# Performance work log

Hardware: AMD Instinct MI355X
Metric: run time of the kernel (lower is better)

## Reference

```python
import jax, jax.numpy as jnp
import numpy as np

NP, NV, S, E = 1500000, 1200000, 50000, 1600000
M, D, C = 32, 64, 20
BN_EPS = 1e-4


def _bn(x, g, be):
    # eval-mode BatchNorm1d with running_mean=0, running_var=1, eps=1e-4
    return x * (g / np.float32(np.sqrt(1.0 + BN_EPS))) + be


def _head(x, W1, b1, g, be, W2, b2):
    # Linear -> BN -> ReLU -> Linear (torch Linear: y = x @ W.T + b)
    h = jax.nn.relu(_bn(x @ W1.T + b1, g, be))
    return h @ W2.T + b2


def setup_inputs() -> dict:
    keys = iter(jax.random.split(jax.random.key(0), 96))
    def nk():
        return next(keys)
    def w(out_d, in_d):
        return (jax.random.normal(nk(), (out_d, in_d), jnp.float32) / np.float32(np.sqrt(in_d)))
    def vec(n, s=0.02):
        return jax.random.normal(nk(), (n,), jnp.float32) * s
    inp = {}
    inp['output_feats'] = jax.random.normal(nk(), (NV, M), jnp.float32)
    inp['input_map'] = jax.random.randint(nk(), (NP,), 0, NV, jnp.int32)
    inp['superpoint'] = jax.random.randint(nk(), (NP,), 0, S, jnp.int32)
    inp['superpoint_center_xyz'] = jax.random.normal(nk(), (S, 3), jnp.float32)
    inp['edge_u'] = jax.random.randint(nk(), (E,), 0, S, jnp.int32)
    inp['edge_v'] = jax.random.randint(nk(), (E,), 0, S, jnp.int32)
    inp['W_ecc'] = w(D, M)
    for pref, din, dout in [('lin', M, C), ('ssem', D, C), ('soff', D, 3), ('socc', D, 1), ('ssize', D, 1), ('feat', D, 7)]:
        inp[pref + '_W1'] = w(din, din)
        inp[pref + '_b1'] = vec(din)
        inp[pref + '_g'] = 1.0 + vec(din, 0.1)
        inp[pref + '_be'] = vec(din, 0.1)
        inp[pref + '_W2'] = w(dout, din)
        inp[pref + '_b2'] = vec(dout)
    inp['pos_W1'] = w(16, 3)
    inp['pos_b1'] = vec(16)
    inp['pos_W2'] = w(1, 16)
    inp['pos_b2'] = vec(1)
    inp['Wq'] = w(D, D)
    inp['Wk'] = w(D, D)
    inp['Wv'] = w(D, D)
    return inp


def reference(output_feats, input_map, superpoint, superpoint_center_xyz, edge_u, edge_v, W_ecc,
              lin_W1, lin_b1, lin_g, lin_be, lin_W2, lin_b2,
              ssem_W1, ssem_b1, ssem_g, ssem_be, ssem_W2, ssem_b2,
              soff_W1, soff_b1, soff_g, soff_be, soff_W2, soff_b2,
              socc_W1, socc_b1, socc_g, socc_be, socc_W2, socc_b2,
              ssize_W1, ssize_b1, ssize_g, ssize_be, ssize_W2, ssize_b2,
              feat_W1, feat_b1, feat_g, feat_be, feat_W2, feat_b2,
              pos_W1, pos_b1, pos_W2, pos_b2, Wq, Wk, Wv):
    nseg = superpoint_center_xyz.shape[0]
    # voxel -> point gather
    pts = output_feats[input_map]                                   # [Np, M]
    semantic_scores = _head(pts, lin_W1, lin_b1, lin_g, lin_be, lin_W2, lin_b2)  # [Np, C]
    # scatter-mean point features into superpoint embeddings
    cnt = jax.ops.segment_sum(jnp.ones((pts.shape[0],), pts.dtype), superpoint, num_segments=nseg)
    emb = jax.ops.segment_sum(pts, superpoint, num_segments=nseg) / jnp.maximum(cnt, 1.0)[:, None]  # [S, M]
    # ECC graph network stand-in: linear projection media -> 64
    ecc = emb @ W_ecc.T                                             # [S, D]
    sp_sem = _head(ecc, ssem_W1, ssem_b1, ssem_g, ssem_be, ssem_W2, ssem_b2)      # [S, C]
    sp_off = _head(ecc, soff_W1, soff_b1, soff_g, soff_be, soff_W2, soff_b2)      # [S, 3]
    sp_occ = _head(ecc, socc_W1, socc_b1, socc_g, socc_be, socc_W2, socc_b2)[:, 0]  # [S]
    sp_size = _head(ecc, ssize_W1, ssize_b1, ssize_g, ssize_be, ssize_W2, ssize_b2)[:, 0]  # [S]
    # edge attention with segment-wise softmax over destination edge_u
    q = ecc @ Wq.T
    k = ecc @ Wk.T
    v = ecc @ Wv.T
    d = superpoint_center_xyz[edge_u] - superpoint_center_xyz[edge_v]             # [E, 3]
    pos = (jax.nn.relu(d @ pos_W1.T + pos_b1) @ pos_W2.T + pos_b2)[:, 0]          # [E]
    aff = (q[edge_u] * k[edge_v]).sum(-1) / np.float32(np.sqrt(D)) * pos          # [E]
    mx = jax.ops.segment_max(aff, edge_u, num_segments=nseg)
    ex = jnp.exp(aff - mx[edge_u])
    tot = jax.ops.segment_sum(ex, edge_u, num_segments=nseg)
    soft = ex / tot[edge_u]                                                       # [E]
    res = jax.ops.segment_sum(soft[:, None] * v[edge_v], edge_u, num_segments=nseg)  # [S, D]
    sp_feat = ecc + res
    sp_disc = _head(sp_feat, feat_W1, feat_b1, feat_g, feat_be, feat_W2, feat_b2)  # [S, 7]
    return (semantic_scores, sp_sem, sp_off, sp_occ, sp_size, soft, sp_disc)
```

## Files before the change

kernel.cpp:

```cpp
#include <hip/hip_runtime.h>
#include <hip/hip_bf16.h>

#define NP_ 1500000
#define NV_ 1200000
#define S_  50000
#define E_  1600000


__global__ void k_zero(int* a, int* b, int* c, int* d, int n) {
    int i = blockIdx.x * blockDim.x + threadIdx.x;
    if (i < n) { a[i] = 0; b[i] = 0; c[i] = 0; d[i] = 0; }
}

__global__ void k_hist2(const int* __restrict__ sp, int* __restrict__ pcnt,
                        const int* __restrict__ eu, int* __restrict__ ecnt) {
    int i = blockIdx.x * blockDim.x + threadIdx.x;
    if (i < NP_) {
        atomicAdd(&pcnt[sp[i]], 1);
    } else {
        int j = i - NP_;
        if (j < E_) atomicAdd(&ecnt[eu[j]], 1);
    }
}

__global__ void k_scan2(const int* __restrict__ pcnt, int* __restrict__ pstart,
                        const int* __restrict__ ecnt, int* __restrict__ estart) {
    __shared__ int sums[1024];
    const int* cnt = (blockIdx.x == 0) ? pcnt : ecnt;
    int* start = (blockIdx.x == 0) ? pstart : estart;
    const int n = S_;
    int t = threadIdx.x;
    int chunk = (n + 1023) / 1024;
    int lo = t * chunk;
    int hi = lo + chunk; if (hi > n) hi = n;
    int s = 0;
    for (int i = lo; i < hi; i++) s += cnt[i];
    sums[t] = s;
    __syncthreads();
    for (int off = 1; off < 1024; off <<= 1) {
        int v = (t >= off) ? sums[t - off] : 0;
        __syncthreads();
        sums[t] += v;
        __syncthreads();
    }
    int run = sums[t] - s;
    for (int i = lo; i < hi; i++) { start[i] = run; run += cnt[i]; }
    if (t == 1023) start[n] = run;
}

__global__ void k_fill2(const int* __restrict__ sp, const int* __restrict__ imap,
                        const int* __restrict__ pstart, int* __restrict__ pcur,
                        int* __restrict__ vidx,
                        const int* __restrict__ eu, const int* __restrict__ ev,
                        const int* __restrict__ estart, int* __restrict__ ecur,
                        int* __restrict__ elist, int* __restrict__ evsarr,
                        const float* __restrict__ ctr,
                        const float* __restrict__ pw1, const float* __restrict__ pb1,
                        const float* __restrict__ pw2, const float* __restrict__ pb2,
                        float* __restrict__ posv) {
    int i = blockIdx.x * blockDim.x + threadIdx.x;
    if (i < NP_) {
        int s = sp[i];
        int off = atomicAdd(&pcur[s], 1);
        vidx[pstart[s] + off] = imap[i];
    } else {
        int e = i - NP_;
        if (e < E_) {
            int u = eu[e], w = ev[e];
            int off = atomicAdd(&ecur[u], 1);
            int r = estart[u] + off;
            elist[r] = e;
            evsarr[r] = w;
            float dx = ctr[u * 3]     - ctr[w * 3];
            float dy = ctr[u * 3 + 1] - ctr[w * 3 + 1];
            float dz = ctr[u * 3 + 2] - ctr[w * 3 + 2];
            float pos = pb2[0];
            #pragma unroll
            for (int hh = 0; hh < 16; hh++) {
                float aa = pb1[hh] + dx * pw1[hh * 3] + dy * pw1[hh * 3 + 1] + dz * pw1[hh * 3 + 2];
                pos += fmaxf(aa, 0.0f) * pw2[hh];
            }
            posv[r] = pos;
        }
    }
}


__global__ __launch_bounds__(256, 4) void k_point_head(
    const float* __restrict__ feats, const int* __restrict__ imap,
    const float* __restrict__ W1, const float* __restrict__ b1,
    const float* __restrict__ g, const float* __restrict__ be,
    const float* __restrict__ W2, const float* __restrict__ b2,
    float* __restrict__ out, int n)
{
    int p = blockIdx.x * 256 + threadIdx.x;
    if (p >= n) return;
    const float4* src = (const float4*)(feats + (size_t)imap[p] * 32);
    float x[32];
    #pragma unroll
    for (int i = 0; i < 8; i++) {
        float4 t = src[i];
        x[i * 4] = t.x; x[i * 4 + 1] = t.y; x[i * 4 + 2] = t.z; x[i * 4 + 3] = t.w;
    }
    float o[20];
    #pragma unroll
    for (int c = 0; c < 20; c++) o[c] = b2[c];
    #pragma unroll
    for (int j = 0; j < 32; j++) {
        float a = b1[j];
        #pragma unroll
        for (int i = 0; i < 32; i++) a = fmaf(x[i], W1[j * 32 + i], a);
        a = a * (g[j] * 0.9999500037f) + be[j];
        a = fmaxf(a, 0.0f);
        #pragma unroll
        for (int c = 0; c < 20; c++) o[c] = fmaf(a, W2[c * 32 + j], o[c]);
    }
    float4* dst = (float4*)(out + (size_t)p * 20);
    #pragma unroll
    for (int i = 0; i < 5; i++) {
        float4 o4;
        o4.x = o[i * 4]; o4.y = o[i * 4 + 1]; o4.z = o[i * 4 + 2]; o4.w = o[i * 4 + 3];
        dst[i] = o4;
    }
}


__global__ __launch_bounds__(256) void k_mean(
    const float* __restrict__ feats, const int* __restrict__ vidx,
    const int* __restrict__ start, float* __restrict__ emb)
{
    int t = blockIdx.x * 256 + threadIdx.x;
    int s = t >> 5, d = t & 31;
    if (s >= S_) return;
    int beg = start[s], end = start[s + 1];
    float acc = 0.0f;
    int i = beg;
    for (; i + 4 <= end; i += 4) {
        int p0 = vidx[i], p1 = vidx[i + 1], p2 = vidx[i + 2], p3 = vidx[i + 3];
        float f0 = feats[(size_t)p0 * 32 + d];
        float f1 = feats[(size_t)p1 * 32 + d];
        float f2 = feats[(size_t)p2 * 32 + d];
        float f3 = feats[(size_t)p3 * 32 + d];
        acc += f0 + f1 + f2 + f3;
    }
    for (; i < end; i++) acc += feats[(size_t)vidx[i] * 32 + d];
    float c = (float)(end - beg);
    emb[(size_t)s * 32 + d] = acc / fmaxf(c, 1.0f);
}


__global__ __launch_bounds__(256) void k_ecc(
    const float* __restrict__ emb, const float* __restrict__ Wecc, float* __restrict__ ecc)
{
    __shared__ float WL[64 * 33];
    int tid = threadIdx.x;
    for (int idx = tid; idx < 64 * 32; idx += 256) WL[(idx >> 5) * 33 + (idx & 31)] = Wecc[idx];
    __syncthreads();
    int w = tid >> 6, j = tid & 63;
    for (int s0 = blockIdx.x * 4 + w; s0 < S_; s0 += gridDim.x * 4) {
        int s = __builtin_amdgcn_readfirstlane(s0);
        const float* x = emb + (size_t)s * 32;
        float a = 0.0f;
        #pragma unroll
        for (int i = 0; i < 32; i++) a = fmaf(x[i], WL[j * 33 + i], a);
        ecc[(size_t)s * 64 + j] = a;
    }
}


__global__ __launch_bounds__(256) void k_qkv(
    const float* __restrict__ ecc,
    const float* __restrict__ Wq, const float* __restrict__ Wk, const float* __restrict__ Wv,
    float* __restrict__ q, float* __restrict__ k, float* __restrict__ v)
{
    __shared__ float QL[64 * 65], KL[64 * 65], VL[64 * 65];
    int tid = threadIdx.x;
    for (int idx = tid; idx < 4096; idx += 256) {
        int r = idx >> 6, c = idx & 63;
        QL[r * 65 + c] = Wq[idx]; KL[r * 65 + c] = Wk[idx]; VL[r * 65 + c] = Wv[idx];
    }
    __syncthreads();
    int w = tid >> 6, j = tid & 63;
    for (int s0 = blockIdx.x * 4 + w; s0 < S_; s0 += gridDim.x * 4) {
        int s = __builtin_amdgcn_readfirstlane(s0);
        const float* x = ecc + (size_t)s * 64;
        float aq = 0.0f, ak = 0.0f, av = 0.0f;
        #pragma unroll
        for (int i = 0; i < 64; i++) {
            float xi = x[i];
            aq = fmaf(xi, QL[j * 65 + i], aq);
            ak = fmaf(xi, KL[j * 65 + i], ak);
            av = fmaf(xi, VL[j * 65 + i], av);
        }
        q[(size_t)s * 64 + j] = aq;
        k[(size_t)s * 64 + j] = ak;
        v[(size_t)s * 64 + j] = av;
    }
}


__global__ __launch_bounds__(256) void k_head(
    const float* __restrict__ in,
    const float* __restrict__ W1, const float* __restrict__ b1,
    const float* __restrict__ g, const float* __restrict__ be,
    const float* __restrict__ W2, const float* __restrict__ b2,
    float* __restrict__ out, int C)
{
    __shared__ float W1L[64 * 65];
    __shared__ float W2L[20 * 65];
    __shared__ float b1L[64], sL[64], beL[64], b2L[20];
    __shared__ float hbuf[4][64];
    int tid = threadIdx.x;
    for (int idx = tid; idx < 4096; idx += 256) W1L[(idx >> 6) * 65 + (idx & 63)] = W1[idx];
    for (int idx = tid; idx < C * 64; idx += 256) W2L[(idx >> 6) * 65 + (idx & 63)] = W2[idx];
    if (tid < 64) { b1L[tid] = b1[tid]; sL[tid] = g[tid] * 0.9999500037f; beL[tid] = be[tid]; }
    if (tid < C) b2L[tid] = b2[tid];
    __syncthreads();
    int w = tid >> 6, lane = tid & 63;
    for (int s0 = blockIdx.x * 4 + w; s0 < S_; s0 += gridDim.x * 4) {
        int s = __builtin_amdgcn_readfirstlane(s0);
        const float* x = in + (size_t)s * 64;
        float a = b1L[lane];
        #pragma unroll
        for (int i = 0; i < 64; i++) a = fmaf(x[i], W1L[lane * 65 + i], a);
        a = a * sL[lane] + beL[lane];
        float h = fmaxf(a, 0.0f);
        hbuf[w][lane] = h;
        if (lane < C) {
            float acc = b2L[lane];
            #pragma unroll
            for (int j = 0; j < 64; j++) acc = fmaf(hbuf[w][j], W2L[lane * 65 + j], acc);
            out[(size_t)s * C + lane] = acc;
        }
    }
}


__global__ __launch_bounds__(256) void k_attn(
    const int* __restrict__ start, const int* __restrict__ list,
    const int* __restrict__ evs, const float* __restrict__ posv,
    const float* __restrict__ q, const float* __restrict__ k,
    const float* __restrict__ v, const float* __restrict__ ecc,
    float* __restrict__ affs, float* __restrict__ soft, float* __restrict__ featb)
{
    int t = blockIdx.x * 256 + threadIdx.x;
    int s0 = t >> 6, lane = t & 63;
    if (s0 >= S_) return;
    int s = __builtin_amdgcn_readfirstlane(s0);
    int beg = start[s], end = start[s + 1];
    float qv = q[(size_t)s * 64 + lane];

    float m = -3.0e38f;
    int r = beg;
    for (; r + 8 <= end; r += 8) {
        float p[8];
        #pragma unroll
        for (int u = 0; u < 8; u++) p[u] = qv * k[(size_t)evs[r + u] * 64 + lane];
        #pragma unroll
        for (int o = 32; o; o >>= 1) {
            #pragma unroll
            for (int u = 0; u < 8; u++) p[u] += __shfl_xor(p[u], o, 64);
        }
        float a[8];
        #pragma unroll
        for (int u = 0; u < 8; u++) { a[u] = p[u] * 0.125f * posv[r + u]; m = fmaxf(m, a[u]); }
        float av = a[0];
        #pragma unroll
        for (int u = 1; u < 8; u++) av = (lane == u) ? a[u] : av;
        if (lane < 8) affs[r + lane] = av;
    }
    for (; r < end; r++) {
        float p = qv * k[(size_t)evs[r] * 64 + lane];
        #pragma unroll
        for (int o = 32; o; o >>= 1) p += __shfl_xor(p, o, 64);
        float a = p * 0.125f * posv[r];
        m = fmaxf(m, a);
        if (lane == 0) affs[r] = a;
    }

    float tot = 0.0f;
    for (int i = beg + lane; i < end; i += 64) tot += __expf(affs[i] - m);
    #pragma unroll
    for (int o = 32; o; o >>= 1) tot += __shfl_xor(tot, o, 64);
    float inv = tot > 0.0f ? 1.0f / tot : 0.0f;

    float r0 = 0.0f, r1 = 0.0f, r2 = 0.0f, r3 = 0.0f;
    int i = beg;
    for (; i + 8 <= end; i += 8) {
        float sv[8];
        #pragma unroll
        for (int u = 0; u < 8; u++) sv[u] = __expf(affs[i + u] - m) * inv;
        float vv[8];
        #pragma unroll
        for (int u = 0; u < 8; u++) vv[u] = v[(size_t)evs[i + u] * 64 + lane];
        r0 = fmaf(sv[0], vv[0], r0); r1 = fmaf(sv[1], vv[1], r1);
        r2 = fmaf(sv[2], vv[2], r2); r3 = fmaf(sv[3], vv[3], r3);
        r0 = fmaf(sv[4], vv[4], r0); r1 = fmaf(sv[5], vv[5], r1);
        r2 = fmaf(sv[6], vv[6], r2); r3 = fmaf(sv[7], vv[7], r3);
        float ssel = sv[0];
        #pragma unroll
        for (int u = 1; u < 8; u++) ssel = (lane == u) ? sv[u] : ssel;
        if (lane < 8) soft[list[i + lane]] = ssel;
    }
    for (; i < end; i++) {
        float sf = __expf(affs[i] - m) * inv;
        r0 = fmaf(sf, v[(size_t)evs[i] * 64 + lane], r0);
        if (lane == 0) soft[list[i]] = sf;
    }
    float res = (r0 + r1) + (r2 + r3);
    featb[(size_t)s * 64 + lane] = ecc[(size_t)s * 64 + lane] + res;
}


extern "C" void kernel_launch(void* const* d_in, const int* in_sizes, int n_in,
                              void* d_out, int out_size, void* d_ws, size_t ws_size,
                              hipStream_t stream) {
    const float* output_feats = (const float*)d_in[0];
    const int*   input_map    = (const int*)d_in[1];
    const int*   superpoint   = (const int*)d_in[2];
    const float* ctr          = (const float*)d_in[3];
    const int*   edge_u       = (const int*)d_in[4];
    const int*   edge_v       = (const int*)d_in[5];
    const float* W_ecc        = (const float*)d_in[6];
    const float* lin_W1 = (const float*)d_in[7];
    const float* lin_b1 = (const float*)d_in[8];
    const float* lin_g  = (const float*)d_in[9];
    const float* lin_be = (const float*)d_in[10];
    const float* lin_W2 = (const float*)d_in[11];
    const float* lin_b2 = (const float*)d_in[12];
    const float* pos_W1 = (const float*)d_in[43];
    const float* pos_b1 = (const float*)d_in[44];
    const float* pos_W2 = (const float*)d_in[45];
    const float* pos_b2 = (const float*)d_in[46];
    const float* Wq     = (const float*)d_in[47];
    const float* Wk     = (const float*)d_in[48];
    const float* Wv     = (const float*)d_in[49];

    float* out = (float*)d_out;
    float* o_sem    = out;
    float* o_spsem  = out + 30000000;
    float* o_spoff  = out + 31000000;
    float* o_spocc  = out + 31150000;
    float* o_spsize = out + 31200000;
    float* o_soft   = out + 31250000;
    float* o_spdisc = out + 32850000;

    char* base = (char*)d_ws;
    size_t off = 0;
    auto alloc = [&](size_t bytes) -> char* {
        char* p = base + off;
        off = (off + bytes + 255) & ~(size_t)255;
        return p;
    };
    int*   pt_cnt   = (int*)alloc(S_ * 4);
    int*   pt_start = (int*)alloc((S_ + 1) * 4);
    int*   pt_cur   = (int*)alloc(S_ * 4);
    int*   vidx     = (int*)alloc((size_t)NP_ * 4);
    int*   e_cnt    = (int*)alloc(S_ * 4);
    int*   e_start  = (int*)alloc((S_ + 1) * 4);
    int*   e_cur    = (int*)alloc(S_ * 4);
    int*   e_list   = (int*)alloc((size_t)E_ * 4);
    int*   e_vs     = (int*)alloc((size_t)E_ * 4);
    float* affs     = (float*)alloc((size_t)E_ * 4);
    float* posv     = (float*)alloc((size_t)E_ * 4);
    float* emb      = (float*)alloc((size_t)S_ * 32 * 4);
    float* ecc      = (float*)alloc((size_t)S_ * 64 * 4);
    float* qb       = (float*)alloc((size_t)S_ * 64 * 4);
    float* kb       = (float*)alloc((size_t)S_ * 64 * 4);
    float* vb       = (float*)alloc((size_t)S_ * 64 * 4);
    float* featb    = qb;

    const int NTOT = NP_ + E_;

    k_zero<<<(S_ + 255) / 256, 256, 0, stream>>>(pt_cnt, pt_cur, e_cnt, e_cur, S_);
    k_hist2<<<(NTOT + 255) / 256, 256, 0, stream>>>(superpoint, pt_cnt, edge_u, e_cnt);
    k_scan2<<<2, 1024, 0, stream>>>(pt_cnt, pt_start, e_cnt, e_start);
    k_fill2<<<(NTOT + 255) / 256, 256, 0, stream>>>(
        superpoint, input_map, pt_start, pt_cur, vidx,
        edge_u, edge_v, e_start, e_cur, e_list, e_vs,
        ctr, pos_W1, pos_b1, pos_W2, pos_b2, posv);
    k_point_head<<<(NP_ + 255) / 256, 256, 0, stream>>>(
        output_feats, input_map, lin_W1, lin_b1, lin_g, lin_be, lin_W2, lin_b2, o_sem, NP_);
    k_mean<<<(S_ * 32) / 256, 256, 0, stream>>>(output_feats, vidx, pt_start, emb);
    k_ecc<<<1024, 256, 0, stream>>>(emb, W_ecc, ecc);
    k_qkv<<<768, 256, 0, stream>>>(ecc, Wq, Wk, Wv, qb, kb, vb);
    k_head<<<1024, 256, 0, stream>>>(ecc, (const float*)d_in[13], (const float*)d_in[14],
        (const float*)d_in[15], (const float*)d_in[16], (const float*)d_in[17], (const float*)d_in[18],
        o_spsem, 20);
    k_head<<<1024, 256, 0, stream>>>(ecc, (const float*)d_in[19], (const float*)d_in[20],
        (const float*)d_in[21], (const float*)d_in[22], (const float*)d_in[23], (const float*)d_in[24],
        o_spoff, 3);
    k_head<<<1024, 256, 0, stream>>>(ecc, (const float*)d_in[25], (const float*)d_in[26],
        (const float*)d_in[27], (const float*)d_in[28], (const float*)d_in[29], (const float*)d_in[30],
        o_spocc, 1);
    k_head<<<1024, 256, 0, stream>>>(ecc, (const float*)d_in[31], (const float*)d_in[32],
        (const float*)d_in[33], (const float*)d_in[34], (const float*)d_in[35], (const float*)d_in[36],
        o_spsize, 1);
    k_attn<<<S_ / 4, 256, 0, stream>>>(e_start, e_list, e_vs, posv, qb, kb, vb, ecc,
        affs, o_soft, featb);
    k_head<<<1024, 256, 0, stream>>>(featb, (const float*)d_in[37], (const float*)d_in[38],
        (const float*)d_in[39], (const float*)d_in[40], (const float*)d_in[41], (const float*)d_in[42],
        o_spdisc, 7);
}
```

Baseline: 1.167 ms.

## Restructure CSR build, per-thread superpoint matmuls, fused heads and online-softmax attention

The histogram pass now records each element's atomic rank, so the fill pass can scatter without a second set of atomics or cursor arrays. The ecc, qkv and head kernels change from one wave per superpoint with LDS weights to one thread per superpoint, reading weights as uniform loads. The four ecc heads are fused into one kernel, and k and v are interleaved into a single buffer. Attention uses an online softmax that builds the weighted v sum in the first pass, which removes the second gather pass over v. The risks are high register pressure in the per-thread kernels, less parallelism at only about 782 blocks of 64 threads, and the rank array aliasing the emb buffer.

```diff
diff --git a/kernel.cpp b/kernel.cpp
--- a/kernel.cpp
+++ b/kernel.cpp
@@ -1,5 +1,4 @@
 #include <hip/hip_runtime.h>
-#include <hip/hip_bf16.h>
 
 #define NP_ 1500000
 #define NV_ 1200000
@@ -7,19 +6,21 @@
 #define E_  1600000
 
 
-__global__ void k_zero(int* a, int* b, int* c, int* d, int n) {
+__global__ void k_zero2(int* a, int* b, int n) {
     int i = blockIdx.x * blockDim.x + threadIdx.x;
-    if (i < n) { a[i] = 0; b[i] = 0; c[i] = 0; d[i] = 0; }
-}
-
-__global__ void k_hist2(const int* __restrict__ sp, int* __restrict__ pcnt,
-                        const int* __restrict__ eu, int* __restrict__ ecnt) {
-    int i = blockIdx.x * blockDim.x + threadIdx.x;
+    if (i < n) { a[i] = 0; b[i] = 0; }
+}
+
+__global__ __launch_bounds__(256) void k_rank(
+    const int* __restrict__ sp, int* __restrict__ pcnt,
+    const int* __restrict__ eu, int* __restrict__ ecnt,
+    int* __restrict__ rank)
+{
+    int i = blockIdx.x * 256 + threadIdx.x;
     if (i < NP_) {
-        atomicAdd(&pcnt[sp[i]], 1);
-    } else {
-        int j = i - NP_;
-        if (j < E_) atomicAdd(&ecnt[eu[j]], 1);
+        rank[i] = atomicAdd(&pcnt[sp[i]], 1);
+    } else if (i < NP_ + E_) {
+        rank[i] = atomicAdd(&ecnt[eu[i - NP_]], 1);
     }
 }
 
@@ -48,40 +49,37 @@
     if (t == 1023) start[n] = run;
 }
 
-__global__ void k_fill2(const int* __restrict__ sp, const int* __restrict__ imap,
-                        const int* __restrict__ pstart, int* __restrict__ pcur,
-                        int* __restrict__ vidx,
-                        const int* __restrict__ eu, const int* __restrict__ ev,
-                        const int* __restrict__ estart, int* __restrict__ ecur,
-                        int* __restrict__ elist, int* __restrict__ evsarr,
-                        const float* __restrict__ ctr,
-                        const float* __restrict__ pw1, const float* __restrict__ pb1,
-                        const float* __restrict__ pw2, const float* __restrict__ pb2,
-                        float* __restrict__ posv) {
-    int i = blockIdx.x * blockDim.x + threadIdx.x;
+__global__ __launch_bounds__(256) void k_scatter(
+    const int* __restrict__ sp, const int* __restrict__ imap,
+    const int* __restrict__ pstart, int* __restrict__ vidx,
+    const int* __restrict__ eu, const int* __restrict__ ev,
+    const int* __restrict__ estart,
+    int* __restrict__ elist, int* __restrict__ evsarr,
+    const int* __restrict__ rank,
+    const float* __restrict__ ctr,
+    const float* __restrict__ pw1, const float* __restrict__ pb1,
+    const float* __restrict__ pw2, const float* __restrict__ pb2,
+    float* __restrict__ posv)
+{
+    int i = blockIdx.x * 256 + threadIdx.x;
     if (i < NP_) {
-        int s = sp[i];
-        int off = atomicAdd(&pcur[s], 1);
-        vidx[pstart[s] + off] = imap[i];
-    } else {
+        vidx[pstart[sp[i]] + rank[i]] = imap[i];
+    } else if (i < NP_ + E_) {
         int e = i - NP_;
-        if (e < E_) {
-            int u = eu[e], w = ev[e];
-            int off = atomicAdd(&ecur[u], 1);
-            int r = estart[u] + off;
-            elist[r] = e;
-            evsarr[r] = w;
-            float dx = ctr[u * 3]     - ctr[w * 3];
-            float dy = ctr[u * 3 + 1] - ctr[w * 3 + 1];
-            float dz = ctr[u * 3 + 2] - ctr[w * 3 + 2];
-            float pos = pb2[0];
-            #pragma unroll
-            for (int hh = 0; hh < 16; hh++) {
-                float aa = pb1[hh] + dx * pw1[hh * 3] + dy * pw1[hh * 3 + 1] + dz * pw1[hh * 3 + 2];
-                pos += fmaxf(aa, 0.0f) * pw2[hh];
-            }
-            posv[r] = pos;
-        }
+        int u = eu[e], w = ev[e];
+        int r = estart[u] + rank[i];
+        elist[r] = e;
+        evsarr[r] = w;
+        float dx = ctr[u * 3]     - ctr[w * 3];
+        float dy = ctr[u * 3 + 1] - ctr[w * 3 + 1];
+        float dz = ctr[u * 3 + 2] - ctr[w * 3 + 2];
+        float pos = pb2[0];
+        #pragma unroll
+        for (int hh = 0; hh < 16; hh++) {
+            float aa = pb1[hh] + dx * pw1[hh * 3] + dy * pw1[hh * 3 + 1] + dz * pw1[hh * 3 + 2];
+            pos += fmaxf(aa, 0.0f) * pw2[hh];
+        }
+        posv[r] = pos;
     }
 }
 
@@ -149,98 +147,170 @@
 }
 
 
-__global__ __launch_bounds__(256) void k_ecc(
+__global__ __launch_bounds__(64) void k_ecc(
     const float* __restrict__ emb, const float* __restrict__ Wecc, float* __restrict__ ecc)
 {
-    __shared__ float WL[64 * 33];
-    int tid = threadIdx.x;
-    for (int idx = tid; idx < 64 * 32; idx += 256) WL[(idx >> 5) * 33 + (idx & 31)] = Wecc[idx];
-    __syncthreads();
-    int w = tid >> 6, j = tid & 63;
-    for (int s0 = blockIdx.x * 4 + w; s0 < S_; s0 += gridDim.x * 4) {
-        int s = __builtin_amdgcn_readfirstlane(s0);
-        const float* x = emb + (size_t)s * 32;
-        float a = 0.0f;
-        #pragma unroll
-        for (int i = 0; i < 32; i++) a = fmaf(x[i], WL[j * 33 + i], a);
-        ecc[(size_t)s * 64 + j] = a;
-    }
-}
-
-
-__global__ __launch_bounds__(256) void k_qkv(
+    int s = blockIdx.x * 64 + threadIdx.x;
+    if (s >= S_) return;
+    float x[32];
+    const float4* src = (const float4*)(emb + (size_t)s * 32);
+    #pragma unroll
+    for (int i = 0; i < 8; i++) {
+        float4 t = src[i];
+        x[i * 4] = t.x; x[i * 4 + 1] = t.y; x[i * 4 + 2] = t.z; x[i * 4 + 3] = t.w;
+    }
+    for (int j0 = 0; j0 < 64; j0 += 4) {
+        float a[4] = {0.f, 0.f, 0.f, 0.f};
+        #pragma unroll
+        for (int u = 0; u < 4; u++)
+            #pragma unroll
+            for (int i = 0; i < 32; i++) a[u] = fmaf(x[i], Wecc[(j0 + u) * 32 + i], a[u]);
+        float4 o4; o4.x = a[0]; o4.y = a[1]; o4.z = a[2]; o4.w = a[3];
+        *(float4*)(ecc + (size_t)s * 64 + j0) = o4;
+    }
+}
+
+
+__global__ __launch_bounds__(64) void k_qkv(
     const float* __restrict__ ecc,
     const float* __restrict__ Wq, const float* __restrict__ Wk, const float* __restrict__ Wv,
-    float* __restrict__ q, float* __restrict__ k, float* __restrict__ v)
-{
-    __shared__ float QL[64 * 65], KL[64 * 65], VL[64 * 65];
-    int tid = threadIdx.x;
-    for (int idx = tid; idx < 4096; idx += 256) {
-        int r = idx >> 6, c = idx & 63;
-        QL[r * 65 + c] = Wq[idx]; KL[r * 65 + c] = Wk[idx]; VL[r * 65 + c] = Wv[idx];
-    }
-    __syncthreads();
-    int w = tid >> 6, j = tid & 63;
-    for (int s0 = blockIdx.x * 4 + w; s0 < S_; s0 += gridDim.x * 4) {
-        int s = __builtin_amdgcn_readfirstlane(s0);
-        const float* x = ecc + (size_t)s * 64;
-        float aq = 0.0f, ak = 0.0f, av = 0.0f;
+    float* __restrict__ q, float* __restrict__ kv)
+{
+    int s = blockIdx.x * 64 + threadIdx.x;
+    if (s >= S_) return;
+    float x[64];
+    const float4* src = (const float4*)(ecc + (size_t)s * 64);
+    #pragma unroll
+    for (int i = 0; i < 16; i++) {
+        float4 t = src[i];
+        x[i * 4] = t.x; x[i * 4 + 1] = t.y; x[i * 4 + 2] = t.z; x[i * 4 + 3] = t.w;
+    }
+    for (int j0 = 0; j0 < 64; j0 += 4) {
+        float aq[4] = {0.f, 0.f, 0.f, 0.f};
+        float ak[4] = {0.f, 0.f, 0.f, 0.f};
+        float av[4] = {0.f, 0.f, 0.f, 0.f};
+        #pragma unroll
+        for (int u = 0; u < 4; u++) {
+            #pragma unroll
+            for (int i = 0; i < 64; i++) {
+                float xi = x[i];
+                aq[u] = fmaf(xi, Wq[(j0 + u) * 64 + i], aq[u]);
+                ak[u] = fmaf(xi, Wk[(j0 + u) * 64 + i], ak[u]);
+                av[u] = fmaf(xi, Wv[(j0 + u) * 64 + i], av[u]);
+            }
+        }
+        float4 t;
+        t.x = aq[0]; t.y = aq[1]; t.z = aq[2]; t.w = aq[3];
+        *(float4*)(q + (size_t)s * 64 + j0) = t;
+        t.x = ak[0]; t.y = ak[1]; t.z = ak[2]; t.w = ak[3];
+        *(float4*)(kv + (size_t)s * 128 + j0) = t;
+        t.x = av[0]; t.y = av[1]; t.z = av[2]; t.w = av[3];
+        *(float4*)(kv + (size_t)s * 128 + 64 + j0) = t;
+    }
+}
+
+
+__global__ __launch_bounds__(64) void k_heads4(
+    const float* __restrict__ ecc,
+    const float* __restrict__ W1s, const float* __restrict__ b1s, const float* __restrict__ gs,
+    const float* __restrict__ bes, const float* __restrict__ W2s, const float* __restrict__ b2s,
+    const float* __restrict__ W1o, const float* __restrict__ b1o, const float* __restrict__ go,
+    const float* __restrict__ beo, const float* __restrict__ W2o, const float* __restrict__ b2o,
+    const float* __restrict__ W1c, const float* __restrict__ b1c, const float* __restrict__ gc,
+    const float* __restrict__ bec, const float* __restrict__ W2c, const float* __restrict__ b2c,
+    const float* __restrict__ W1z, const float* __restrict__ b1z, const float* __restrict__ gz,
+    const float* __restrict__ bez, const float* __restrict__ W2z, const float* __restrict__ b2z,
+    float* __restrict__ osem, float* __restrict__ ooff,
+    float* __restrict__ oocc, float* __restrict__ osiz)
+{
+    int s = blockIdx.x * 64 + threadIdx.x;
+    if (s >= S_) return;
+    float x[64];
+    const float4* src = (const float4*)(ecc + (size_t)s * 64);
+    #pragma unroll
+    for (int i = 0; i < 16; i++) {
+        float4 t = src[i];
+        x[i * 4] = t.x; x[i * 4 + 1] = t.y; x[i * 4 + 2] = t.z; x[i * 4 + 3] = t.w;
+    }
+    float as[20], ao[3], ac, az;
+    #pragma unroll
+    for (int c = 0; c < 20; c++) as[c] = b2s[c];
+    #pragma unroll
+    for (int c = 0; c < 3; c++) ao[c] = b2o[c];
+    ac = b2c[0]; az = b2z[0];
+    for (int j = 0; j < 64; j++) {
+        float h0 = b1s[j], h1 = b1o[j], h2 = b1c[j], h3 = b1z[j];
         #pragma unroll
         for (int i = 0; i < 64; i++) {
             float xi = x[i];
-            aq = fmaf(xi, QL[j * 65 + i], aq);
-            ak = fmaf(xi, KL[j * 65 + i], ak);
-            av = fmaf(xi, VL[j * 65 + i], av);
-        }
-        q[(size_t)s * 64 + j] = aq;
-        k[(size_t)s * 64 + j] = ak;
-        v[(size_t)s * 64 + j] = av;
-    }
-}
-
-
-__global__ __launch_bounds__(256) void k_head(
+            h0 = fmaf(xi, W1s[j * 64 + i], h0);
+            h1 = fmaf(xi, W1o[j * 64 + i], h1);
+            h2 = fmaf(xi, W1c[j * 64 + i], h2);
+            h3 = fmaf(xi, W1z[j * 64 + i], h3);
+        }
+        h0 = fmaxf(h0 * (gs[j] * 0.9999500037f) + bes[j], 0.f);
+        h1 = fmaxf(h1 * (go[j] * 0.9999500037f) + beo[j], 0.f);
+        h2 = fmaxf(h2 * (gc[j] * 0.9999500037f) + bec[j], 0.f);
+        h3 = fmaxf(h3 * (gz[j] * 0.9999500037f) + bez[j], 0.f);
+        #pragma unroll
+        for (int c = 0; c < 20; c++) as[c] = fmaf(h0, W2s[c * 64 + j], as[c]);
+        #pragma unroll
+        for (int c = 0; c < 3; c++) ao[c] = fmaf(h1, W2o[c * 64 + j], ao[c]);
+        ac = fmaf(h2, W2c[j], ac);
+        az = fmaf(h3, W2z[j], az);
+    }
+    float4* d = (float4*)(osem + (size_t)s * 20);
+    #pragma unroll
+    for (int i = 0; i < 5; i++) {
+        float4 o4;
+        o4.x = as[i * 4]; o4.y = as[i * 4 + 1]; o4.z = as[i * 4 + 2]; o4.w = as[i * 4 + 3];
+        d[i] = o4;
+    }
+    ooff[(size_t)s * 3]     = ao[0];
+    ooff[(size_t)s * 3 + 1] = ao[1];
+    ooff[(size_t)s * 3 + 2] = ao[2];
+    oocc[s] = ac;
+    osiz[s] = az;
+}
+
+
+__global__ __launch_bounds__(64) void k_featd(
     const float* __restrict__ in,
     const float* __restrict__ W1, const float* __restrict__ b1,
     const float* __restrict__ g, const float* __restrict__ be,
     const float* __restrict__ W2, const float* __restrict__ b2,
-    float* __restrict__ out, int C)
-{
-    __shared__ float W1L[64 * 65];
-    __shared__ float W2L[20 * 65];
-    __shared__ float b1L[64], sL[64], beL[64], b2L[20];
-    __shared__ float hbuf[4][64];
-    int tid = threadIdx.x;
-    for (int idx = tid; idx < 4096; idx += 256) W1L[(idx >> 6) * 65 + (idx & 63)] = W1[idx];
-    for (int idx = tid; idx < C * 64; idx += 256) W2L[(idx >> 6) * 65 + (idx & 63)] = W2[idx];
-    if (tid < 64) { b1L[tid] = b1[tid]; sL[tid] = g[tid] * 0.9999500037f; beL[tid] = be[tid]; }
-    if (tid < C) b2L[tid] = b2[tid];
-    __syncthreads();
-    int w = tid >> 6, lane = tid & 63;
-    for (int s0 = blockIdx.x * 4 + w; s0 < S_; s0 += gridDim.x * 4) {
-        int s = __builtin_amdgcn_readfirstlane(s0);
-        const float* x = in + (size_t)s * 64;
-        float a = b1L[lane];
-        #pragma unroll
-        for (int i = 0; i < 64; i++) a = fmaf(x[i], W1L[lane * 65 + i], a);
-        a = a * sL[lane] + beL[lane];
-        float h = fmaxf(a, 0.0f);
-        hbuf[w][lane] = h;
-        if (lane < C) {
-            float acc = b2L[lane];
-            #pragma unroll
-            for (int j = 0; j < 64; j++) acc = fmaf(hbuf[w][j], W2L[lane * 65 + j], acc);
-            out[(size_t)s * C + lane] = acc;
-        }
-    }
+    float* __restrict__ out)
+{
+    int s = blockIdx.x * 64 + threadIdx.x;
+    if (s >= S_) return;
+    float x[64];
+    const float4* src = (const float4*)(in + (size_t)s * 64);
+    #pragma unroll
+    for (int i = 0; i < 16; i++) {
+        float4 t = src[i];
+        x[i * 4] = t.x; x[i * 4 + 1] = t.y; x[i * 4 + 2] = t.z; x[i * 4 + 3] = t.w;
+    }
+    float o[7];
+    #pragma unroll
+    for (int c = 0; c < 7; c++) o[c] = b2[c];
+    for (int j = 0; j < 64; j++) {
+        float a = b1[j];
+        #pragma unroll
+        for (int i = 0; i < 64; i++) a = fmaf(x[i], W1[j * 64 + i], a);
+        a = fmaxf(a * (g[j] * 0.9999500037f) + be[j], 0.f);
+        #pragma unroll
+        for (int c = 0; c < 7; c++) o[c] = fmaf(a, W2[c * 64 + j], o[c]);
+    }
+    #pragma unroll
+    for (int c = 0; c < 7; c++) out[(size_t)s * 7 + c] = o[c];
 }
 
 
 __global__ __launch_bounds__(256) void k_attn(
     const int* __restrict__ start, const int* __restrict__ list,
     const int* __restrict__ evs, const float* __restrict__ posv,
-    const float* __restrict__ q, const float* __restrict__ k,
-    const float* __restrict__ v, const float* __restrict__ ecc,
+    const float* __restrict__ q, const float* __restrict__ kv,
+    const float* __restrict__ ecc,
     float* __restrict__ affs, float* __restrict__ soft, float* __restrict__ featb)
 {
     int t = blockIdx.x * 256 + threadIdx.x;
@@ -250,65 +320,65 @@
     int beg = start[s], end = start[s + 1];
     float qv = q[(size_t)s * 64 + lane];
 
-    float m = -3.0e38f;
+    float m = -3.0e38f, tot = 0.0f, res = 0.0f;
     int r = beg;
     for (; r + 8 <= end; r += 8) {
+        int e[8];
+        #pragma unroll
+        for (int u = 0; u < 8; u++) e[u] = evs[r + u];
+        float kk[8], vv[8];
+        #pragma unroll
+        for (int u = 0; u < 8; u++) {
+            const float* row = kv + (size_t)e[u] * 128;
+            kk[u] = row[lane];
+            vv[u] = row[64 + lane];
+        }
         float p[8];
         #pragma unroll
-        for (int u = 0; u < 8; u++) p[u] = qv * k[(size_t)evs[r + u] * 64 + lane];
+        for (int u = 0; u < 8; u++) p[u] = qv * kk[u];
         #pragma unroll
         for (int o = 32; o; o >>= 1) {
             #pragma unroll
             for (int u = 0; u < 8; u++) p[u] += __shfl_xor(p[u], o, 64);
         }
         float a[8];
-        #pragma unroll
-        for (int u = 0; u < 8; u++) { a[u] = p[u] * 0.125f * posv[r + u]; m = fmaxf(m, a[u]); }
+        float cm = -3.0e38f;
+        #pragma unroll
+        for (int u = 0; u < 8; u++) { a[u] = p[u] * 0.125f * posv[r + u]; cm = fmaxf(cm, a[u]); }
+        float mn = fmaxf(m, cm);
+        float scale = __expf(m - mn);
+        res *= scale; tot *= scale; m = mn;
+        #pragma unroll
+        for (int u = 0; u < 8; u++) {
+            float w = __expf(a[u] - m);
+            tot += w;
+            res = fmaf(w, vv[u], res);
+        }
         float av = a[0];
         #pragma unroll
         for (int u = 1; u < 8; u++) av = (lane == u) ? a[u] : av;
         if (lane < 8) affs[r + lane] = av;
     }
     for (; r < end; r++) {
-        float p = qv * k[(size_t)evs[r] * 64 + lane];
+        const float* row = kv + (size_t)evs[r] * 128;
+        float kk = row[lane], vv = row[64 + lane];
+        float p = qv * kk;
         #pragma unroll
         for (int o = 32; o; o >>= 1) p += __shfl_xor(p, o, 64);
         float a = p * 0.125f * posv[r];
-        m = fmaxf(m, a);
+        float mn = fmaxf(m, a);
+        float scale = __expf(m - mn);
+        res *= scale; tot *= scale; m = mn;
+        float w = __expf(a - m);
+        tot += w;
+        res = fmaf(w, vv, res);
         if (lane == 0) affs[r] = a;
     }
-
-    float tot = 0.0f;
-    for (int i = beg + lane; i < end; i += 64) tot += __expf(affs[i] - m);
-    #pragma unroll
-    for (int o = 32; o; o >>= 1) tot += __shfl_xor(tot, o, 64);
     float inv = tot > 0.0f ? 1.0f / tot : 0.0f;
 
-    float r0 = 0.0f, r1 = 0.0f, r2 = 0.0f, r3 = 0.0f;
-    int i = beg;
-    for (; i + 8 <= end; i += 8) {
-        float sv[8];
-        #pragma unroll
-        for (int u = 0; u < 8; u++) sv[u] = __expf(affs[i + u] - m) * inv;
-        float vv[8];
-        #pragma unroll
-        for (int u = 0; u < 8; u++) vv[u] = v[(size_t)evs[i + u] * 64 + lane];
-        r0 = fmaf(sv[0], vv[0], r0); r1 = fmaf(sv[1], vv[1], r1);
-        r2 = fmaf(sv[2], vv[2], r2); r3 = fmaf(sv[3], vv[3], r3);
-        r0 = fmaf(sv[4], vv[4], r0); r1 = fmaf(sv[5], vv[5], r1);
-        r2 = fmaf(sv[6], vv[6], r2); r3 = fmaf(sv[7], vv[7], r3);
-        float ssel = sv[0];
-        #pragma unroll
-        for (int u = 1; u < 8; u++) ssel = (lane == u) ? sv[u] : ssel;
-        if (lane < 8) soft[list[i + lane]] = ssel;
-    }
-    for (; i < end; i++) {
-        float sf = __expf(affs[i] - m) * inv;
-        r0 = fmaf(sf, v[(size_t)evs[i] * 64 + lane], r0);
-        if (lane == 0) soft[list[i]] = sf;
-    }
-    float res = (r0 + r1) + (r2 + r3);
-    featb[(size_t)s * 64 + lane] = ecc[(size_t)s * 64 + lane] + res;
+    for (int i = beg + lane; i < end; i += 64) soft[list[i]] = __expf(affs[i] - m) * inv;
+
+    featb[(size_t)s * 64 + lane] = ecc[(size_t)s * 64 + lane] + res * inv;
 }
 
 
@@ -354,11 +424,9 @@
     };
     int*   pt_cnt   = (int*)alloc(S_ * 4);
     int*   pt_start = (int*)alloc((S_ + 1) * 4);
-    int*   pt_cur   = (int*)alloc(S_ * 4);
-    int*   vidx     = (int*)alloc((size_t)NP_ * 4);
     int*   e_cnt    = (int*)alloc(S_ * 4);
     int*   e_start  = (int*)alloc((S_ + 1) * 4);
-    int*   e_cur    = (int*)alloc(S_ * 4);
+    int*   vidx     = (int*)alloc((size_t)NP_ * 4);
     int*   e_list   = (int*)alloc((size_t)E_ * 4);
     int*   e_vs     = (int*)alloc((size_t)E_ * 4);
     float* affs     = (float*)alloc((size_t)E_ * 4);
@@ -366,39 +434,38 @@
     float* emb      = (float*)alloc((size_t)S_ * 32 * 4);
     float* ecc      = (float*)alloc((size_t)S_ * 64 * 4);
     float* qb       = (float*)alloc((size_t)S_ * 64 * 4);
-    float* kb       = (float*)alloc((size_t)S_ * 64 * 4);
-    float* vb       = (float*)alloc((size_t)S_ * 64 * 4);
+    float* kvb      = (float*)alloc((size_t)S_ * 128 * 4);
     float* featb    = qb;
+    int*   rank     = (int*)emb;
 
     const int NTOT = NP_ + E_;
 
-    k_zero<<<(S_ + 255) / 256, 256, 0, stream>>>(pt_cnt, pt_cur, e_cnt, e_cur, S_);
-    k_hist2<<<(NTOT + 255) / 256, 256, 0, stream>>>(superpoint, pt_cnt, edge_u, e_cnt);
+    k_zero2<<<(S_ + 255) / 256, 256, 0, stream>>>(pt_cnt, e_cnt, S_);
+    k_rank<<<(NTOT + 255) / 256, 256, 0, stream>>>(superpoint, pt_cnt, edge_u, e_cnt, rank);
     k_scan2<<<2, 1024, 0, stream>>>(pt_cnt, pt_start, e_cnt, e_start);
-    k_fill2<<<(NTOT + 255) / 256, 256, 0, stream>>>(
-        superpoint, input_map, pt_start, pt_cur, vidx,
-        edge_u, edge_v, e_start, e_cur, e_list, e_vs,
+    k_scatter<<<(NTOT + 255) / 256, 256, 0, stream>>>(
+        superpoint, input_map, pt_start, vidx,
+        edge_u, edge_v, e_start, e_list, e_vs, rank,
         ctr, pos_W1, pos_b1, pos_W2, pos_b2, posv);
     k_point_head<<<(NP_ + 255) / 256, 256, 0, stream>>>(
         output_feats, input_map, lin_W1, lin_b1, lin_g, lin_be, lin_W2, lin_b2, o_sem, NP_);
     k_mean<<<(S_ * 32) / 256, 256, 0, stream>>>(output_feats, vidx, pt_start, emb);
-    k_ecc<<<1024, 256, 0, stream>>>(emb, W_ecc, ecc);
-    k_qkv<<<768, 256, 0, stream>>>(ecc, Wq, Wk, Wv, qb, kb, vb);
-    k_head<<<1024, 256, 0, stream>>>(ecc, (const float*)d_in[13], (const float*)d_in[14],
-        (const float*)d_in[15], (const float*)d_in[16], (const float*)d_in[17], (const float*)d_in[18],
-        o_spsem, 20);
-    k_head<<<1024, 256, 0, stream>>>(ecc, (const float*)d_in[19], (const float*)d_in[20],
-        (const float*)d_in[21], (const float*)d_in[22], (const float*)d_in[23], (const float*)d_in[24],
-        o_spoff, 3);
-    k_head<<<1024, 256, 0, stream>>>(ecc, (const float*)d_in[25], (const float*)d_in[26],
-        (const float*)d_in[27], (const float*)d_in[28], (const float*)d_in[29], (const float*)d_in[30],
-        o_spocc, 1);
-    k_head<<<1024, 256, 0, stream>>>(ecc, (const float*)d_in[31], (const float*)d_in[32],
-        (const float*)d_in[33], (const float*)d_in[34], (const float*)d_in[35], (const float*)d_in[36],
-        o_spsize, 1);
-    k_attn<<<S_ / 4, 256, 0, stream>>>(e_start, e_list, e_vs, posv, qb, kb, vb, ecc,
+    k_ecc<<<(S_ + 63) / 64, 64, 0, stream>>>(emb, W_ecc, ecc);
+    k_qkv<<<(S_ + 63) / 64, 64, 0, stream>>>(ecc, Wq, Wk, Wv, qb, kvb);
+    k_heads4<<<(S_ + 63) / 64, 64, 0, stream>>>(ecc,
+        (const float*)d_in[13], (const float*)d_in[14], (const float*)d_in[15],
+        (const float*)d_in[16], (const float*)d_in[17], (const float*)d_in[18],
+        (const float*)d_in[19], (const float*)d_in[20], (const float*)d_in[21],
+        (const float*)d_in[22], (const float*)d_in[23], (const float*)d_in[24],
+        (const float*)d_in[25], (const float*)d_in[26], (const float*)d_in[27],
+        (const float*)d_in[28], (const float*)d_in[29], (const float*)d_in[30],
+        (const float*)d_in[31], (const float*)d_in[32], (const float*)d_in[33],
+        (const float*)d_in[34], (const float*)d_in[35], (const float*)d_in[36],
+        o_spsem, o_spoff, o_spocc, o_spsize);
+    k_attn<<<S_ / 4, 256, 0, stream>>>(e_start, e_list, e_vs, posv, qb, kvb, ecc,
         affs, o_soft, featb);
-    k_head<<<1024, 256, 0, stream>>>(featb, (const float*)d_in[37], (const float*)d_in[38],
-        (const float*)d_in[39], (const float*)d_in[40], (const float*)d_in[41], (const float*)d_in[42],
-        o_spdisc, 7);
-}
+    k_featd<<<(S_ + 63) / 64, 64, 0, stream>>>(featb,
+        (const float*)d_in[37], (const float*)d_in[38], (const float*)d_in[39],
+        (const float*)d_in[40], (const float*)d_in[41], (const float*)d_in[42],
+        o_spdisc);
+}
```

Result: slower. 1.500 ms (+28.6%).
